# Kernel tuning notes

Measured on AMD Instinct MI355X. Metric: run time of the kernel, lower is better.

The kernel has to match this reference:

```python
import jax, jax.numpy as jnp
import numpy as np

SHAPES = [(100, 168), (50, 84), (25, 42)]  # per-level (h, w)
HEADS, LEVELS, POINTS, EMBED = 8, 3, 8, 256
D_ANCHORS = 4  # num_Z_anchors; POINTS % D_ANCHORS == 0


def _bilinear_sample(v_l, loc, h, w):
    # v_l: [B, H, h*w, d]; loc: [B, nq, H, P, 2] normalized sampling locations
    B, nq, H, P, _ = loc.shape
    d = v_l.shape[-1]
    # F.grid_sample(align_corners=False, padding_mode='zeros'): pixel = loc*size - 0.5
    x = loc[..., 0] * w - 0.5
    y = loc[..., 1] * h - 0.5
    x0 = jnp.floor(x)
    y0 = jnp.floor(y)
    lx = x - x0
    ly = y - y0
    x0 = x0.astype(jnp.int32)
    y0 = y0.astype(jnp.int32)

    def gather(xi, yi):
        valid = ((xi >= 0) & (xi < w) & (yi >= 0) & (yi < h)).astype(v_l.dtype)
        idx = jnp.clip(yi, 0, h - 1) * w + jnp.clip(xi, 0, w - 1)  # [B,nq,H,P]
        idx = jnp.transpose(idx, (0, 2, 1, 3)).reshape(B, H, nq * P)
        vals = jnp.take_along_axis(v_l, idx[..., None], axis=2)  # [B,H,nq*P,d]
        vals = jnp.transpose(vals.reshape(B, H, nq, P, d), (0, 2, 1, 3, 4))
        return vals * valid[..., None]

    v00 = gather(x0, y0)
    v10 = gather(x0 + 1, y0)
    v01 = gather(x0, y0 + 1)
    v11 = gather(x0 + 1, y0 + 1)
    wx, wy = lx[..., None], ly[..., None]
    return (v00 * (1 - wx) * (1 - wy) + v10 * wx * (1 - wy)
            + v01 * (1 - wx) * wy + v11 * wx * wy)


def _msda(q, v, ref, Wv, bv, Ws, b_off, Wa, ba):
    # MSDeformableAttention3D: q [B,nq,C], v [B,nv,C], ref [B,nq,D,2]
    B, nq, C = q.shape
    nv = v.shape[1]
    d = C // HEADS
    val = (v @ Wv + bv).reshape(B, nv, HEADS, d).transpose(0, 2, 1, 3)  # [B,H,nv,d]
    off = (q @ Ws + b_off).reshape(B, nq, HEADS, LEVELS, POINTS, 2)
    aw = jax.nn.softmax((q @ Wa + ba).reshape(B, nq, HEADS, LEVELS * POINTS), axis=-1)
    aw = aw.reshape(B, nq, HEADS, LEVELS, POINTS)
    norm = jnp.array([[w, h] for (h, w) in SHAPES], dtype=q.dtype)  # offset_normalizer (w,h)
    off = off / norm[None, None, None, :, None, :]
    off = off.reshape(B, nq, HEADS, LEVELS, POINTS // D_ANCHORS, D_ANCHORS, 2)
    loc = ref[:, :, None, None, None, :, :] + off  # sampling_locations
    loc = loc.reshape(B, nq, HEADS, LEVELS, POINTS, 2)
    out = jnp.zeros((B, nq, HEADS, d), q.dtype)
    start = 0
    for lvl, (h, w) in enumerate(SHAPES):
        v_l = val[:, :, start:start + h * w, :]
        start += h * w
        s = _bilinear_sample(v_l, loc[:, :, :, lvl], h, w)  # [B,nq,H,P,d]
        out = out + jnp.einsum('bqhpd,bqhp->bqhd', s, aw[:, :, :, lvl])
    return out.reshape(B, nq, C)


def _forward(query, key, value, query_pos, reference_points_cam, bev_mask,
             Wv, bv, Ws, b_off, Wa, ba, Wo, bo):
    bs, nq, C = query.shape
    ncam = key.shape[0]
    inp_residual = query
    q = query + query_pos
    # key/value: [num_cams, l, bs, C] -> [bs*num_cams, l, C]
    v = jnp.transpose(value, (2, 0, 1, 3)).reshape(bs * ncam, -1, C)
    # dense equivalent of the per-camera query rebatching: run MSDA on all
    # queries per camera, then mask out non-hit queries (identical math)
    qc = jnp.broadcast_to(q[:, None], (bs, ncam, nq, C)).reshape(bs * ncam, nq, C)
    ref = jnp.transpose(reference_points_cam, (1, 0, 2, 3, 4)).reshape(bs * ncam, nq, D_ANCHORS, 2)
    out = _msda(qc, v, ref, Wv, bv, Ws, b_off, Wa, ba).reshape(bs, ncam, nq, C)
    hit = jnp.transpose(bev_mask.sum(-1) > 0, (1, 0, 2)).astype(out.dtype)  # [bs,ncam,nq]
    slots = (out * hit[..., None]).sum(axis=1)
    count = jnp.clip(hit.sum(axis=1), 1.0, None)
    slots = slots / count[..., None]
    slots = slots @ Wo + bo
    return slots + inp_residual  # dropout is identity at inference


def setup_inputs() -> dict:
    key0 = jax.random.key(0)
    ks = jax.random.split(key0, 12)
    bs, ncam, nq = 1, 6, 4096
    nv = sum(h * w for h, w in SHAPES)
    f = jnp.float32
    s = 0.02
    inp = {}
    inp['query'] = jax.random.normal(ks[0], (bs, nq, EMBED), f)
    inp['key'] = jax.random.normal(ks[1], (ncam, nv, bs, EMBED), f)
    inp['value'] = jax.random.normal(ks[2], (ncam, nv, bs, EMBED), f)
    inp['query_pos'] = jax.random.normal(ks[3], (bs, nq, EMBED), f)
    inp['reference_points_cam'] = jax.random.uniform(ks[4], (ncam, bs, nq, D_ANCHORS, 2), f)
    inp['bev_mask'] = jax.random.bernoulli(ks[5], 0.9, (ncam, bs, nq, D_ANCHORS))
    inp['spatial_shapes'] = jnp.array(SHAPES, dtype=jnp.int32)
    inp['level_start_index'] = jnp.array(np.cumsum([0] + [h * w for h, w in SHAPES[:-1]]), dtype=jnp.int32)
    inp['Wv'] = jax.random.normal(ks[6], (EMBED, EMBED), f) * s
    inp['bv'] = jnp.zeros((EMBED,), f)
    inp['Ws'] = jax.random.normal(ks[7], (EMBED, HEADS * LEVELS * POINTS * 2), f) * s
    inp['b_off'] = jax.random.normal(ks[8], (HEADS * LEVELS * POINTS * 2,), f) * 0.5
    inp['Wa'] = jax.random.normal(ks[9], (EMBED, HEADS * LEVELS * POINTS), f) * s
    inp['ba'] = jnp.zeros((HEADS * LEVELS * POINTS,), f)
    inp['Wo'] = jax.random.normal(ks[10], (EMBED, EMBED), f) * s
    inp['bo'] = jnp.zeros((EMBED,), f)
    return inp


def reference(query, key, value, query_pos, reference_points_cam, bev_mask,
              spatial_shapes, level_start_index,
              Wv, bv, Ws, b_off, Wa, ba, Wo, bo):
    return _forward(query, key, value, query_pos, reference_points_cam, bev_mask,
                    Wv, bv, Ws, b_off, Wa, ba, Wo, bo)
```

## Files before the change

kernel.cpp:

```cpp
#include <hip/hip_runtime.h>
#include <stdint.h>

#define NQ 4096
#define NCAM 6
#define NV 22050
#define M_TOTAL (NCAM * NV)

typedef __bf16 bf16x8 __attribute__((ext_vector_type(8)));
typedef float f32x4 __attribute__((ext_vector_type(4)));
typedef unsigned int u32x4 __attribute__((ext_vector_type(4)));

__device__ __forceinline__ unsigned short f2bf(float f) {
    union { float f; uint32_t u; } v; v.f = f;
    uint32_t u = v.u;
    uint32_t r = (u + 0x7FFFu + ((u >> 16) & 1u)) >> 16;
    return (unsigned short)r;
}
__device__ __forceinline__ float bf_lo(uint32_t u) {
    union { uint32_t u; float f; } v; v.u = u << 16; return v.f;
}
__device__ __forceinline__ float bf_hi(uint32_t u) {
    union { uint32_t u; float f; } v; v.u = u & 0xFFFF0000u; return v.f;
}
__device__ __forceinline__ int imin(int a, int b) { return a < b ? a : b; }
__device__ __forceinline__ int imax(int a, int b) { return a > b ? a : b; }

__global__ void wvt_kernel(const float* __restrict__ Wv, unsigned short* __restrict__ WvT) {
    int n = blockIdx.x, k = threadIdx.x;
    WvT[n * 256 + k] = f2bf(Wv[k * 256 + n]);
}

__global__ __launch_bounds__(256) void val_gemm(const float* __restrict__ A,
                                                const unsigned short* __restrict__ BT,
                                                const float* __restrict__ bv,
                                                unsigned short* __restrict__ C) {
    __shared__ unsigned char Asm[64 * 80];
    __shared__ unsigned char Bsm[256 * 80];
    const int t = threadIdx.x;
    const int wave = t >> 6, lane = t & 63;
    const int m_base = blockIdx.x * 64;

    f32x4 acc[4][4];
#pragma unroll
    for (int i = 0; i < 4; ++i)
#pragma unroll
        for (int j = 0; j < 4; ++j) acc[i][j] = (f32x4)0.0f;

    const int rsel = lane & 15, g = lane >> 4;

    for (int k0 = 0; k0 < 256; k0 += 32) {
        __syncthreads();
#pragma unroll
        for (int it = 0; it < 2; ++it) {
            int cc = t + it * 256;
            int r = cc >> 3, ck = cc & 7;
            int gr = imin(m_base + r, M_TOTAL - 1);
            float4 v = *reinterpret_cast<const float4*>(A + (size_t)gr * 256 + k0 + ck * 4);
            uint2 pk;
            pk.x = (uint32_t)f2bf(v.x) | ((uint32_t)f2bf(v.y) << 16);
            pk.y = (uint32_t)f2bf(v.z) | ((uint32_t)f2bf(v.w) << 16);
            *reinterpret_cast<uint2*>(&Asm[r * 80 + ck * 8]) = pk;
        }
#pragma unroll
        for (int it = 0; it < 4; ++it) {
            int cc = t + it * 256;
            int n = cc >> 2, ck = cc & 3;
            u32x4 v = *reinterpret_cast<const u32x4*>(BT + n * 256 + k0 + ck * 8);
            *reinterpret_cast<u32x4*>(&Bsm[n * 80 + ck * 16]) = v;
        }
        __syncthreads();

        bf16x8 af[4], bfr[4];
#pragma unroll
        for (int mi = 0; mi < 4; ++mi)
            af[mi] = __builtin_bit_cast(bf16x8,
                *reinterpret_cast<const u32x4*>(&Asm[(mi * 16 + rsel) * 80 + g * 16]));
#pragma unroll
        for (int ni = 0; ni < 4; ++ni)
            bfr[ni] = __builtin_bit_cast(bf16x8,
                *reinterpret_cast<const u32x4*>(&Bsm[(wave * 64 + ni * 16 + rsel) * 80 + g * 16]));
#pragma unroll
        for (int mi = 0; mi < 4; ++mi)
#pragma unroll
            for (int ni = 0; ni < 4; ++ni)
                acc[mi][ni] = __builtin_amdgcn_mfma_f32_16x16x32_bf16(af[mi], bfr[ni], acc[mi][ni], 0, 0, 0);
    }

#pragma unroll
    for (int ni = 0; ni < 4; ++ni) {
        int n = wave * 64 + ni * 16 + rsel;
        float bvv = bv[n];
        const int hp = n >> 5, ch = n & 31;
#pragma unroll
        for (int mi = 0; mi < 4; ++mi)
#pragma unroll
            for (int j = 0; j < 4; ++j) {
                int m = m_base + mi * 16 + g * 4 + j;
                if (m < M_TOTAL) {
                    unsigned int um = (unsigned int)m;
                    unsigned int c = um / 22050u;
                    unsigned int pix = um - c * 22050u;
                    C[(((size_t)c * 8 + hp) * NV + pix) * 32 + ch] = f2bf(acc[mi][ni][j] + bvv);
                }
            }
    }
}

__global__ __launch_bounds__(256) void proj_kernel(const float* __restrict__ query,
                                                   const float* __restrict__ qpos,
                                                   const float* __restrict__ Ws,
                                                   const float* __restrict__ b_off,
                                                   const float* __restrict__ Wa,
                                                   const float* __restrict__ ba,
                                                   float* __restrict__ off_ws,
                                                   float* __restrict__ aw_ws) {
    __shared__ float qrow[4][256];
    __shared__ float logits[4][192];
    const int t = threadIdx.x;
    const int qb = blockIdx.x * 4;
#pragma unroll
    for (int j = 0; j < 4; ++j)
        qrow[j][t] = query[(size_t)(qb + j) * 256 + t] + qpos[(size_t)(qb + j) * 256 + t];
    __syncthreads();

    const float invn[3][2] = {{1.f / 168.f, 1.f / 100.f},
                              {1.f / 84.f, 1.f / 50.f},
                              {1.f / 42.f, 1.f / 25.f}};
#pragma unroll
    for (int pass = 0; pass < 3; ++pass) {
        int u = t + pass * 256;
        if (u < 384) {
            float a0 = 0.f, a1 = 0.f, a2 = 0.f, a3 = 0.f;
            for (int k = 0; k < 256; ++k) {
                float w = Ws[k * 384 + u];
                a0 += qrow[0][k] * w; a1 += qrow[1][k] * w;
                a2 += qrow[2][k] * w; a3 += qrow[3][k] * w;
            }
            int lp = u >> 1;
            int l = (lp >> 3) % 3;
            float inv = invn[l][u & 1];
            float b = b_off[u];
            off_ws[(size_t)(qb + 0) * 384 + u] = (a0 + b) * inv;
            off_ws[(size_t)(qb + 1) * 384 + u] = (a1 + b) * inv;
            off_ws[(size_t)(qb + 2) * 384 + u] = (a2 + b) * inv;
            off_ws[(size_t)(qb + 3) * 384 + u] = (a3 + b) * inv;
        } else if (u < 576) {
            int u2 = u - 384;
            float a0 = 0.f, a1 = 0.f, a2 = 0.f, a3 = 0.f;
            for (int k = 0; k < 256; ++k) {
                float w = Wa[k * 192 + u2];
                a0 += qrow[0][k] * w; a1 += qrow[1][k] * w;
                a2 += qrow[2][k] * w; a3 += qrow[3][k] * w;
            }
            float b = ba[u2];
            logits[0][u2] = a0 + b; logits[1][u2] = a1 + b;
            logits[2][u2] = a2 + b; logits[3][u2] = a3 + b;
        }
    }
    __syncthreads();
    if (t < 32) {
        int jq = t >> 3, h = t & 7;
        float mx = -1e30f;
#pragma unroll
        for (int i = 0; i < 24; ++i) mx = fmaxf(mx, logits[jq][h * 24 + i]);
        float e[24];
        float s = 0.f;
#pragma unroll
        for (int i = 0; i < 24; ++i) { e[i] = __expf(logits[jq][h * 24 + i] - mx); s += e[i]; }
        float inv = 1.0f / s;
#pragma unroll
        for (int i = 0; i < 24; ++i)
            aw_ws[((size_t)(qb + jq) * 8 + h) * 24 + i] = e[i] * inv;
    }
}

__global__ __launch_bounds__(256) void sample_kernel(const unsigned short* __restrict__ val,
                                                     const float* __restrict__ rpc,
                                                     const float* __restrict__ off_ws,
                                                     const float* __restrict__ aw_ws,
                                                     unsigned short* __restrict__ out_cam) {
    const int t = threadIdx.x;
    const int qs = t >> 2;
    const int sub = t & 3;
    const int p = blockIdx.x;
    const int x = p & 7;
    const int g = x + 8 * (p >> 9);
    const int wblk = (p >> 3) & 63;
    const int c = g >> 3, h = g & 7;
    const int q = wblk * 64 + qs;
    const int pair = c * NQ + q;

    float refx[4], refy[4];
    const float* rp = rpc + (size_t)pair * 8;
#pragma unroll
    for (int a = 0; a < 4; ++a) { refx[a] = rp[2 * a]; refy[a] = rp[2 * a + 1]; }

    const unsigned short* vbase = val + (size_t)g * NV * 32 + sub * 8;
    const float* offp = off_ws + (size_t)q * 384 + h * 48;
    const float* awp = aw_ws + ((size_t)q * 8 + h) * 24;

    float acc[8];
#pragma unroll
    for (int i = 0; i < 8; ++i) acc[i] = 0.f;

    const int lw[3] = {168, 84, 42};
    const int lhh[3] = {100, 50, 25};
    const int lst[3] = {0, 16800, 21000};

#pragma unroll
    for (int l = 0; l < 3; ++l) {
        const int w = lw[l], hh = lhh[l];
        const float wf = (float)w, hf = (float)hh;
        const unsigned short* vlev = vbase + (size_t)lst[l] * 32;
#pragma unroll
        for (int pt = 0; pt < 8; ++pt) {
            const int a = pt & 3;
            float ox = offp[(l * 8 + pt) * 2 + 0];
            float oy = offp[(l * 8 + pt) * 2 + 1];
            float xx = fmaf(refx[a] + ox, wf, -0.5f);
            float yy = fmaf(refy[a] + oy, hf, -0.5f);
            float xf = floorf(xx), yf = floorf(yy);
            float lx = xx - xf, ly = yy - yf;
            int x0 = (int)xf, y0 = (int)yf;
            float aww = awp[l * 8 + pt];

            float wx0 = (x0 >= 0 && x0 < w) ? (1.f - lx) : 0.f;
            float wx1 = (x0 >= -1 && x0 < w - 1) ? lx : 0.f;
            float wy0 = ((y0 >= 0 && y0 < hh) ? (1.f - ly) : 0.f) * aww;
            float wy1 = ((y0 >= -1 && y0 < hh - 1) ? ly : 0.f) * aww;

            int x0c = imin(imax(x0, 0), w - 1);
            int x1c = imin(imax(x0 + 1, 0), w - 1);
            int y0c = imin(imax(y0, 0), hh - 1);
            int y1c = imin(imax(y0 + 1, 0), hh - 1);

            int r0 = y0c * w, r1 = y1c * w;
            u32x4 u00 = *reinterpret_cast<const u32x4*>(vlev + (size_t)(r0 + x0c) * 32);
            u32x4 u10 = *reinterpret_cast<const u32x4*>(vlev + (size_t)(r0 + x1c) * 32);
            u32x4 u01 = *reinterpret_cast<const u32x4*>(vlev + (size_t)(r1 + x0c) * 32);
            u32x4 u11 = *reinterpret_cast<const u32x4*>(vlev + (size_t)(r1 + x1c) * 32);

            float w00 = wx0 * wy0, w10 = wx1 * wy0, w01 = wx0 * wy1, w11 = wx1 * wy1;
#pragma unroll
            for (int i = 0; i < 4; ++i) {
                acc[2 * i] += w00 * bf_lo(u00[i]) + w10 * bf_lo(u10[i]) +
                              w01 * bf_lo(u01[i]) + w11 * bf_lo(u11[i]);
                acc[2 * i + 1] += w00 * bf_hi(u00[i]) + w10 * bf_hi(u10[i]) +
                                  w01 * bf_hi(u01[i]) + w11 * bf_hi(u11[i]);
            }
        }
    }

    u32x4 o;
#pragma unroll
    for (int i = 0; i < 4; ++i)
        o[i] = (uint32_t)f2bf(acc[2 * i]) | ((uint32_t)f2bf(acc[2 * i + 1]) << 16);
    *reinterpret_cast<u32x4*>(out_cam + (size_t)pair * 256 + h * 32 + sub * 8) = o;
}

__global__ __launch_bounds__(256) void combine_kernel(const unsigned short* __restrict__ out_cam,
                                                      const unsigned char* __restrict__ bev_mask,
                                                      const float* __restrict__ Wo,
                                                      const float* __restrict__ bo,
                                                      const float* __restrict__ query,
                                                      float* __restrict__ out) {
    __shared__ float s_lds[8][256];
    __shared__ unsigned int hitm[8];
    __shared__ float invc[8];
    const int t = threadIdx.x;
    const int qb = blockIdx.x * 8;

    if (t < 8) {
        int q = qb + t;
        unsigned int m = 0;
        int cnt = 0;
        for (int c = 0; c < 6; ++c) {
            const unsigned char* bm = bev_mask + ((size_t)c * NQ + q) * 4;
            if (bm[0] | bm[1] | bm[2] | bm[3]) { m |= (1u << c); cnt++; }
        }
        hitm[t] = m;
        invc[t] = 1.0f / (float)imax(cnt, 1);
    }
    __syncthreads();
#pragma unroll
    for (int j = 0; j < 8; ++j) {
        unsigned int m = hitm[j];
        float ic = invc[j];
        float s = 0.f;
#pragma unroll
        for (int c = 0; c < 6; ++c)
            if ((m >> c) & 1u) {
                unsigned short u = out_cam[((size_t)c * NQ + qb + j) * 256 + t];
                union { uint32_t u; float f; } v; v.u = ((uint32_t)u) << 16;
                s += v.f;
            }
        s_lds[j][t] = s * ic;
    }
    __syncthreads();
    float acc[8] = {0.f, 0.f, 0.f, 0.f, 0.f, 0.f, 0.f, 0.f};
    for (int k = 0; k < 256; ++k) {
        float wv = Wo[k * 256 + t];
#pragma unroll
        for (int j = 0; j < 8; ++j) acc[j] += s_lds[j][k] * wv;
    }
    float bb = bo[t];
#pragma unroll
    for (int j = 0; j < 8; ++j)
        out[(size_t)(qb + j) * 256 + t] = acc[j] + bb + query[(size_t)(qb + j) * 256 + t];
}

extern "C" void kernel_launch(void* const* d_in, const int* in_sizes, int n_in,
                              void* d_out, int out_size, void* d_ws, size_t ws_size,
                              hipStream_t stream) {
    const float* query = (const float*)d_in[0];
    const float* value = (const float*)d_in[2];
    const float* qpos = (const float*)d_in[3];
    const float* rpc = (const float*)d_in[4];
    const unsigned char* bev = (const unsigned char*)d_in[5];
    const float* Wv = (const float*)d_in[8];
    const float* bv = (const float*)d_in[9];
    const float* Ws = (const float*)d_in[10];
    const float* b_off = (const float*)d_in[11];
    const float* Wa = (const float*)d_in[12];
    const float* ba = (const float*)d_in[13];
    const float* Wo = (const float*)d_in[14];
    const float* bo = (const float*)d_in[15];
    float* out = (float*)d_out;

    char* ws = (char*)d_ws;
    unsigned short* val_ws = (unsigned short*)ws;
    size_t o = 67737600;
    float* off_ws = (float*)(ws + o);            o += 6291456;
    float* aw_ws = (float*)(ws + o);             o += 3145728;
    unsigned short* out_cam = (unsigned short*)(ws + o); o += 12582912;
    unsigned short* WvT = (unsigned short*)(ws + o);

    wvt_kernel<<<256, 256, 0, stream>>>(Wv, WvT);
    proj_kernel<<<NQ / 4, 256, 0, stream>>>(query, qpos, Ws, b_off, Wa, ba, off_ws, aw_ws);
    val_gemm<<<(M_TOTAL + 63) / 64, 256, 0, stream>>>(value, WvT, bv, val_ws);
    sample_kernel<<<3072, 256, 0, stream>>>(val_ws, rpc, off_ws, aw_ws, out_cam);
    combine_kernel<<<NQ / 8, 256, 0, stream>>>(out_cam, bev, Wo, bo, query, out);
}
```

Measured before the change: 223.1 us.

## Load GEMM fragments directly from global and vectorize bf16 output stores

The value-projection GEMM no longer stages A and B tiles through shared memory with barriers. Each lane now loads its MFMA fragments straight from global memory, converting fp32 to bf16 in registers. The MFMA operands are swapped so each lane holds four consecutive output channels, which allows packed 8-byte stores instead of scattered 2-byte stores. The trade-off is less data reuse across waves, since every wave re-reads the A rows, plus uncoalesced per-lane global loads that rely on cache.

```diff
diff --git a/kernel.cpp b/kernel.cpp
--- a/kernel.cpp
+++ b/kernel.cpp
@@ -34,10 +34,9 @@
                                                 const unsigned short* __restrict__ BT,
                                                 const float* __restrict__ bv,
                                                 unsigned short* __restrict__ C) {
-    __shared__ unsigned char Asm[64 * 80];
-    __shared__ unsigned char Bsm[256 * 80];
     const int t = threadIdx.x;
-    const int wave = t >> 6, lane = t & 63;
+    const int w = t >> 6, lane = t & 63;
+    const int r = lane & 15, g = lane >> 4;
     const int m_base = blockIdx.x * 64;
 
     f32x4 acc[4][4];
@@ -46,63 +45,63 @@
 #pragma unroll
         for (int j = 0; j < 4; ++j) acc[i][j] = (f32x4)0.0f;
 
-    const int rsel = lane & 15, g = lane >> 4;
-
-    for (int k0 = 0; k0 < 256; k0 += 32) {
-        __syncthreads();
-#pragma unroll
-        for (int it = 0; it < 2; ++it) {
-            int cc = t + it * 256;
-            int r = cc >> 3, ck = cc & 7;
-            int gr = imin(m_base + r, M_TOTAL - 1);
-            float4 v = *reinterpret_cast<const float4*>(A + (size_t)gr * 256 + k0 + ck * 4);
-            uint2 pk;
-            pk.x = (uint32_t)f2bf(v.x) | ((uint32_t)f2bf(v.y) << 16);
-            pk.y = (uint32_t)f2bf(v.z) | ((uint32_t)f2bf(v.w) << 16);
-            *reinterpret_cast<uint2*>(&Asm[r * 80 + ck * 8]) = pk;
-        }
-#pragma unroll
-        for (int it = 0; it < 4; ++it) {
-            int cc = t + it * 256;
-            int n = cc >> 2, ck = cc & 3;
-            u32x4 v = *reinterpret_cast<const u32x4*>(BT + n * 256 + k0 + ck * 8);
-            *reinterpret_cast<u32x4*>(&Bsm[n * 80 + ck * 16]) = v;
-        }
-        __syncthreads();
-
-        bf16x8 af[4], bfr[4];
+    const float* arow[4];
+#pragma unroll
+    for (int mi = 0; mi < 4; ++mi)
+        arow[mi] = A + (size_t)imin(m_base + mi * 16 + r, M_TOTAL - 1) * 256 + g * 8;
+    const unsigned short* brow[4];
+#pragma unroll
+    for (int ni = 0; ni < 4; ++ni)
+        brow[ni] = BT + (size_t)(w * 64 + ni * 16 + r) * 256 + g * 8;
+
+#pragma unroll 2
+    for (int ks = 0; ks < 8; ++ks) {
+        bf16x8 bfrag[4];
+#pragma unroll
+        for (int ni = 0; ni < 4; ++ni)
+            bfrag[ni] = __builtin_bit_cast(bf16x8,
+                *reinterpret_cast<const u32x4*>(brow[ni] + ks * 32));
+        bf16x8 afrag[4];
+#pragma unroll
+        for (int mi = 0; mi < 4; ++mi) {
+            float4 lo = *reinterpret_cast<const float4*>(arow[mi] + ks * 32);
+            float4 hi = *reinterpret_cast<const float4*>(arow[mi] + ks * 32 + 4);
+            bf16x8 av;
+            av[0] = (__bf16)lo.x; av[1] = (__bf16)lo.y;
+            av[2] = (__bf16)lo.z; av[3] = (__bf16)lo.w;
+            av[4] = (__bf16)hi.x; av[5] = (__bf16)hi.y;
+            av[6] = (__bf16)hi.z; av[7] = (__bf16)hi.w;
+            afrag[mi] = av;
+        }
 #pragma unroll
         for (int mi = 0; mi < 4; ++mi)
-            af[mi] = __builtin_bit_cast(bf16x8,
-                *reinterpret_cast<const u32x4*>(&Asm[(mi * 16 + rsel) * 80 + g * 16]));
-#pragma unroll
-        for (int ni = 0; ni < 4; ++ni)
-            bfr[ni] = __builtin_bit_cast(bf16x8,
-                *reinterpret_cast<const u32x4*>(&Bsm[(wave * 64 + ni * 16 + rsel) * 80 + g * 16]));
-#pragma unroll
-        for (int mi = 0; mi < 4; ++mi)
 #pragma unroll
             for (int ni = 0; ni < 4; ++ni)
-                acc[mi][ni] = __builtin_amdgcn_mfma_f32_16x16x32_bf16(af[mi], bfr[ni], acc[mi][ni], 0, 0, 0);
+                acc[mi][ni] = __builtin_amdgcn_mfma_f32_16x16x32_bf16(
+                    bfrag[ni], afrag[mi], acc[mi][ni], 0, 0, 0);
     }
 
 #pragma unroll
     for (int ni = 0; ni < 4; ++ni) {
-        int n = wave * 64 + ni * 16 + rsel;
-        float bvv = bv[n];
-        const int hp = n >> 5, ch = n & 31;
-#pragma unroll
-        for (int mi = 0; mi < 4; ++mi)
-#pragma unroll
-            for (int j = 0; j < 4; ++j) {
-                int m = m_base + mi * 16 + g * 4 + j;
-                if (m < M_TOTAL) {
-                    unsigned int um = (unsigned int)m;
-                    unsigned int c = um / 22050u;
-                    unsigned int pix = um - c * 22050u;
-                    C[(((size_t)c * 8 + hp) * NV + pix) * 32 + ch] = f2bf(acc[mi][ni][j] + bvv);
-                }
-            }
+        const int n0 = w * 64 + ni * 16 + g * 4;
+        const float4 bb = *reinterpret_cast<const float4*>(bv + n0);
+        const int hp = n0 >> 5, cc = n0 & 31;
+#pragma unroll
+        for (int mi = 0; mi < 4; ++mi) {
+            int m = m_base + mi * 16 + r;
+            if (m < M_TOTAL) {
+                unsigned int um = (unsigned int)m;
+                unsigned int c = um / 22050u;
+                unsigned int pix = um - c * 22050u;
+                uint2 pk;
+                pk.x = (uint32_t)f2bf(acc[mi][ni][0] + bb.x) |
+                       ((uint32_t)f2bf(acc[mi][ni][1] + bb.y) << 16);
+                pk.y = (uint32_t)f2bf(acc[mi][ni][2] + bb.z) |
+                       ((uint32_t)f2bf(acc[mi][ni][3] + bb.w) << 16);
+                *reinterpret_cast<uint2*>(
+                    C + (((size_t)c * 8 + hp) * NV + pix) * 32 + cc) = pk;
+            }
+        }
     }
 }
 
```

Result: slower. 267.1 us (+19.7%).
